# Kernel tuning notes

Measured on AMD Instinct MI355X. Metric: run time of the kernel, lower is better.

## Reference

```python
import jax, jax.numpy as jnp
import numpy as np

N = 20000      # total nodes
E = 320000     # edges before self loops
G = 64         # graphs in the batch
H = 8          # attention heads
NEG_SLOPE = 0.2
EPS = 1e-5


def _gatv2(x, src, dst, Wl, bl, Wr, br, att, bias, concat):
    # PyG GATv2Conv: xl = lin_l(x) (source/messages), xr = lin_r(x) (target)
    heads, C = att.shape
    xl = (x @ Wl + bl).reshape(-1, heads, C)
    xr = (x @ Wr + br).reshape(-1, heads, C)
    e = jax.nn.leaky_relu(xl[src] + xr[dst], NEG_SLOPE)          # [E', H, C]
    a = jnp.einsum('ehc,hc->eh', e, att)                          # [E', H]
    amax = jax.ops.segment_max(a, dst, num_segments=N)
    a = jnp.exp(a - amax[dst])
    a = a / jax.ops.segment_sum(a, dst, num_segments=N)[dst]
    out = jax.ops.segment_sum(xl[src] * a[..., None], dst, num_segments=N)
    out = out.reshape(-1, heads * C) if concat else out.mean(axis=1)
    return out + bias


def _graphnorm(x, batch, w, b, ms):
    cnt = jnp.maximum(jax.ops.segment_sum(jnp.ones((x.shape[0],), x.dtype), batch, num_segments=G), 1.0)[:, None]
    mean = jax.ops.segment_sum(x, batch, num_segments=G) / cnt
    out = x - mean[batch] * ms
    var = jax.ops.segment_sum(out * out, batch, num_segments=G) / cnt
    return w * out / jnp.sqrt(var + EPS)[batch] + b


def _mean_pool(x, batch):
    cnt = jnp.maximum(jax.ops.segment_sum(jnp.ones((x.shape[0],), x.dtype), batch, num_segments=G), 1.0)[:, None]
    return jax.ops.segment_sum(x, batch, num_segments=G) / cnt


def setup_inputs():
    key = jax.random.key(0)
    ks = iter(jax.random.split(key, 40))

    def gl(shape, scale=0.05):
        return jax.random.normal(next(ks), shape, jnp.float32) * scale

    inp = {}
    inp['x'] = jax.random.normal(next(ks), (N, 19), jnp.float32)
    inp['edge_index'] = jax.random.randint(next(ks), (2, E), 0, N, jnp.int32)
    inp['batch'] = jnp.sort(jax.random.randint(next(ks), (N,), 0, G, jnp.int32))

    # layer 1: 19 -> (8 heads x 32), concat -> 256
    inp['W1l'] = gl((19, 256)); inp['b1l'] = jnp.zeros((256,), jnp.float32)
    inp['W1r'] = gl((19, 256)); inp['b1r'] = jnp.zeros((256,), jnp.float32)
    inp['att1'] = gl((H, 32)); inp['bias1'] = jnp.zeros((256,), jnp.float32)
    inp['gn1_w'] = jnp.ones((256,), jnp.float32); inp['gn1_b'] = jnp.zeros((256,), jnp.float32); inp['gn1_ms'] = jnp.ones((256,), jnp.float32)

    inp['W2l'] = gl((256, 128)); inp['b2l'] = jnp.zeros((128,), jnp.float32)
    inp['W2r'] = gl((256, 128)); inp['b2r'] = jnp.zeros((128,), jnp.float32)
    inp['att2'] = gl((H, 16)); inp['bias2'] = jnp.zeros((128,), jnp.float32)
    inp['gn2_w'] = jnp.ones((128,), jnp.float32); inp['gn2_b'] = jnp.zeros((128,), jnp.float32); inp['gn2_ms'] = jnp.ones((128,), jnp.float32)

    inp['W3l'] = gl((128, 64)); inp['b3l'] = jnp.zeros((64,), jnp.float32)
    inp['W3r'] = gl((128, 64)); inp['b3r'] = jnp.zeros((64,), jnp.float32)
    inp['att3'] = gl((H, 8)); inp['bias3'] = jnp.zeros((8,), jnp.float32)
    inp['gn3_w'] = jnp.ones((8,), jnp.float32); inp['gn3_b'] = jnp.zeros((8,), jnp.float32); inp['gn3_ms'] = jnp.ones((8,), jnp.float32)

    inp['lin_w'] = gl((8, 4)); inp['lin_b'] = jnp.zeros((4,), jnp.float32)
    return inp


def reference(x, edge_index, batch, W1l, b1l, W1r, b1r, att1, bias1, gn1_w, gn1_b, gn1_ms,
              W2l, b2l, W2r, b2r, att2, bias2, gn2_w, gn2_b, gn2_ms,
              W3l, b3l, W3r, b3r, att3, bias3, gn3_w, gn3_b, gn3_ms, lin_w, lin_b):
    loop = jnp.arange(N, dtype=edge_index.dtype)  # GATv2Conv add_self_loops=True
    src = jnp.concatenate([edge_index[0], loop])
    dst = jnp.concatenate([edge_index[1], loop])

    h = _gatv2(x, src, dst, W1l, b1l, W1r, b1r, att1, bias1, True)
    h = jax.nn.relu(_graphnorm(h, batch, gn1_w, gn1_b, gn1_ms))
    h = _gatv2(h, src, dst, W2l, b2l, W2r, b2r, att2, bias2, True)
    h = jax.nn.relu(_graphnorm(h, batch, gn2_w, gn2_b, gn2_ms))
    h = _gatv2(h, src, dst, W3l, b3l, W3r, b3r, att3, bias3, False)
    h = jax.nn.relu(_graphnorm(h, batch, gn3_w, gn3_b, gn3_ms))

    features = _mean_pool(h, batch)        # [G, 8]
    logits = features @ lin_w + lin_b      # [G, 4]
    return (logits, features)
```

## Files before the change

kernel.cpp:

```cpp
#include <hip/hip_runtime.h>
#include <math.h>

#define NN 20000
#define EE 320000
#define GG 64
#define HH 8
#define EPSV 1e-5f

static inline unsigned int gridFor(long n, int b){ return (unsigned int)((n + b - 1)/b); }

typedef __attribute__((ext_vector_type(8))) short short8;
typedef __attribute__((ext_vector_type(4))) float f32x4;
typedef unsigned short ushort_t;

__global__ void k_deg(const int* __restrict__ edst, int* __restrict__ deg){
    int e = blockIdx.x*blockDim.x + threadIdx.x;
    if (e < EE) atomicAdd(&deg[edst[e]], 1);
}

__global__ void k_scan(const int* __restrict__ deg, int* __restrict__ indptr){
    __shared__ int partial[1024];
    const int CH = (NN + 1023)/1024;
    int t = threadIdx.x;
    int base = t*CH;
    int vals[CH];
    int sum = 0;
    for (int i = 0; i < CH; ++i){
        int v = (base+i < NN) ? deg[base+i] : 0;
        vals[i] = sum; sum += v;
    }
    partial[t] = sum;
    __syncthreads();
    for (int off = 1; off < 1024; off <<= 1){
        int v = (t >= off) ? partial[t-off] : 0;
        __syncthreads();
        partial[t] += v;
        __syncthreads();
    }
    int prefix = (t > 0) ? partial[t-1] : 0;
    for (int i = 0; i < CH; ++i)
        if (base+i < NN) indptr[base+i] = prefix + vals[i];
    if (t == 1023) indptr[NN] = prefix + sum;
}

__global__ void k_scatter(const int* __restrict__ esrc, const int* __restrict__ edst,
                          const int* __restrict__ indptr, int* __restrict__ cursor,
                          int* __restrict__ srclist){
    int e = blockIdx.x*blockDim.x + threadIdx.x;
    if (e >= EE) return;
    int d = edst[e];
    int pos = atomicAdd(&cursor[d], 1);
    srclist[indptr[d] + pos] = esrc[e];
}

__global__ void k_bounds(const int* __restrict__ batch, int* __restrict__ gstart, int* __restrict__ gend){
    int i = blockIdx.x*blockDim.x + threadIdx.x;
    if (i >= NN) return;
    int b = batch[i];
    if (i == 0 || batch[i-1] != b) gstart[b] = i;
    if (i == NN-1 || batch[i+1] != b) gend[b] = i+1;
}

__device__ __forceinline__ float asf(unsigned int u){
    union{unsigned int i; float f;} c; c.i = u; return c.f;
}
__device__ __forceinline__ ushort_t f2bf(float x){
    unsigned u = __float_as_uint(x);
    unsigned r = u + 0x7FFFu + ((u >> 16) & 1u);
    return (ushort_t)(r >> 16);
}
__device__ __forceinline__ void split_bf16(float x, short& hi, short& lo){
    unsigned u = __float_as_uint(x);
    unsigned r = u + 0x7FFFu + ((u >> 16) & 1u);
    hi = (short)(r >> 16);
    float hf = asf(((unsigned)(unsigned short)hi) << 16);
    float res = x - hf;
    unsigned u2 = __float_as_uint(res);
    unsigned r2 = u2 + 0x7FFFu + ((u2 >> 16) & 1u);
    lo = (short)(r2 >> 16);
}

__global__ void k_wprep(const float* __restrict__ Wl, const float* __restrict__ Wr,
                        ushort_t* __restrict__ Whi, ushort_t* __restrict__ Wlo,
                        int K, int Kp, int HC){
    int octs = Kp >> 3;
    int t = blockIdx.x*blockDim.x + threadIdx.x;
    if (t >= 2*HC*octs) return;
    int n = t / octs, ko = t - n*octs;
    int kb = ko*8;
    const float* W = (n < HC) ? (Wl + n) : (Wr + (n - HC));
    short hi[8], lo[8];
    #pragma unroll
    for (int j = 0; j < 8; ++j){
        int k = kb + j;
        float v = (k < K) ? W[(long)k*HC] : 0.f;
        split_bf16(v, hi[j], lo[j]);
    }
    long base = (((long)(n>>4)*(Kp>>5) + (kb>>5))*64 + (n&15) + 16*((kb>>3)&3))*8;
    *(short8*)&Whi[base] = *(short8*)hi;
    *(short8*)&Wlo[base] = *(short8*)lo;
}

template<bool NORM>
__global__ __launch_bounds__(256)
void k_gemm_mfma(const float* __restrict__ h,
                 const ushort_t* __restrict__ Whi, const ushort_t* __restrict__ Wlo,
                 const float* __restrict__ bl, const float* __restrict__ br,
                 const float* __restrict__ gmu, const float* __restrict__ ginv,
                 const float* __restrict__ nw, const float* __restrict__ nb,
                 const int* __restrict__ batch,
                 ushort_t* __restrict__ xlb, float* __restrict__ xr,
                 int K, int Kp, int HC){
    __shared__ short Ahi[64*32], Alo[64*32];
    const int tid  = threadIdx.x;
    const int lane = tid & 63;
    const int wave = tid >> 6;
    const int m0   = blockIdx.x * 64;
    const int n0   = blockIdx.y * 128;
    const int wr   = (wave & 1) * 32;
    const int wcg  = (wave >> 1) * 64;
    const int kblocks = Kp >> 5;

    const int srow = tid >> 2;
    const int soct = tid & 3;

    f32x4 acc[2][4] = {};

    for (int kb = 0; kb < kblocks; ++kb){
        int k0 = kb*32;
        {
            int gm = m0 + srow;
            int kbase = k0 + soct*8;
            float v[8];
            const float* src = h + (long)gm*K + kbase;
            if (gm < NN && kbase + 8 <= K){
                float4 t0 = *(const float4*)src;
                float4 t1 = *(const float4*)(src+4);
                v[0]=t0.x; v[1]=t0.y; v[2]=t0.z; v[3]=t0.w;
                v[4]=t1.x; v[5]=t1.y; v[6]=t1.z; v[7]=t1.w;
            } else {
                #pragma unroll
                for (int j = 0; j < 8; ++j)
                    v[j] = (gm < NN && kbase + j < K) ? src[j] : 0.f;
            }
            if (NORM && gm < NN){
                int g = batch[gm];
                const float* mu = gmu + (long)g*K;
                const float* iv = ginv + (long)g*K;
                #pragma unroll
                for (int j = 0; j < 8; ++j){
                    int c = kbase + j;
                    float t = (v[j] - mu[c]) * iv[c] * nw[c] + nb[c];
                    v[j] = fmaxf(t, 0.f);
                }
            }
            short hi[8], lo[8];
            #pragma unroll
            for (int j = 0; j < 8; ++j) split_bf16(v[j], hi[j], lo[j]);
            long off = ((long)(srow>>4)*64 + (srow&15) + 16*soct)*8;
            *(short8*)&Ahi[off] = *(short8*)hi;
            *(short8*)&Alo[off] = *(short8*)lo;
        }
        __syncthreads();

        int rb0 = wr >> 4;
        short8 ah0 = *(short8*)&Ahi[((rb0  )*64 + lane)*8];
        short8 ah1 = *(short8*)&Ahi[((rb0+1)*64 + lane)*8];
        short8 al0 = *(short8*)&Alo[((rb0  )*64 + lane)*8];
        short8 al1 = *(short8*)&Alo[((rb0+1)*64 + lane)*8];

        short8 bh[4], bl_[4];
        #pragma unroll
        for (int j = 0; j < 4; ++j){
            int n = n0 + wcg + j*16;
            long bbase = (((long)(n>>4)*kblocks + kb)*64 + lane)*8;
            bh[j]  = *(const short8*)&Whi[bbase];
            bl_[j] = *(const short8*)&Wlo[bbase];
        }

        #pragma unroll
        for (int j = 0; j < 4; ++j){
            acc[0][j] = __builtin_amdgcn_mfma_f32_16x16x32_bf16(al0, bh[j],  acc[0][j], 0,0,0);
            acc[0][j] = __builtin_amdgcn_mfma_f32_16x16x32_bf16(ah0, bl_[j], acc[0][j], 0,0,0);
            acc[0][j] = __builtin_amdgcn_mfma_f32_16x16x32_bf16(ah0, bh[j],  acc[0][j], 0,0,0);
            acc[1][j] = __builtin_amdgcn_mfma_f32_16x16x32_bf16(al1, bh[j],  acc[1][j], 0,0,0);
            acc[1][j] = __builtin_amdgcn_mfma_f32_16x16x32_bf16(ah1, bl_[j], acc[1][j], 0,0,0);
            acc[1][j] = __builtin_amdgcn_mfma_f32_16x16x32_bf16(ah1, bh[j],  acc[1][j], 0,0,0);
        }
        __syncthreads();
    }

    #pragma unroll
    for (int i = 0; i < 2; ++i){
        int row0 = m0 + wr + i*16 + (lane >> 4)*4;
        #pragma unroll
        for (int j = 0; j < 4; ++j){
            int n = n0 + wcg + j*16 + (lane & 15);
            float bb = (n < HC) ? bl[n] : br[n - HC];
            #pragma unroll
            for (int r = 0; r < 4; ++r){
                int gm = row0 + r;
                if (gm >= NN) continue;
                float v = acc[i][j][r] + bb;
                if (n < HC) xlb[(long)gm*HC + n] = f2bf(v);
                else        xr[(long)gm*HC + (n - HC)] = v;
            }
        }
    }
}

template<int VEC> struct VT;
template<> struct VT<1>{ using T = float;  };
template<> struct VT<2>{ using T = float2; };
template<> struct VT<4>{ using T = float4; };

template<int VEC> struct BF;
template<> struct BF<1>{
    static __device__ __forceinline__ float load(const ushort_t* p){
        return asf(((unsigned)*p) << 16);
    }
};
template<> struct BF<2>{
    static __device__ __forceinline__ float2 load(const ushort_t* p){
        unsigned u = *(const unsigned*)p;
        return make_float2(asf(u << 16), asf(u & 0xFFFF0000u));
    }
};
template<> struct BF<4>{
    static __device__ __forceinline__ float4 load(const ushort_t* p){
        uint2 u = *(const uint2*)p;
        return make_float4(asf(u.x << 16), asf(u.x & 0xFFFF0000u),
                           asf(u.y << 16), asf(u.y & 0xFFFF0000u));
    }
};

__device__ __forceinline__ float lrelu(float z){ return z > 0.f ? z : 0.2f*z; }

__device__ __forceinline__ float edot(float xv, float xr, float at){
    return lrelu(xv + xr) * at;
}
__device__ __forceinline__ float edot(float2 xv, float2 xr, float2 at){
    return lrelu(xv.x+xr.x)*at.x + lrelu(xv.y+xr.y)*at.y;
}
__device__ __forceinline__ float edot(float4 xv, float4 xr, float4 at){
    return lrelu(xv.x+xr.x)*at.x + lrelu(xv.y+xr.y)*at.y
         + lrelu(xv.z+xr.z)*at.z + lrelu(xv.w+xr.w)*at.w;
}
__device__ __forceinline__ void efma(float& o, float p, float xv){ o = fmaf(p,xv,o); }
__device__ __forceinline__ void efma(float2& o, float p, float2 xv){
    o.x = fmaf(p,xv.x,o.x); o.y = fmaf(p,xv.y,o.y);
}
__device__ __forceinline__ void efma(float4& o, float p, float4 xv){
    o.x = fmaf(p,xv.x,o.x); o.y = fmaf(p,xv.y,o.y);
    o.z = fmaf(p,xv.z,o.z); o.w = fmaf(p,xv.w,o.w);
}
__device__ __forceinline__ float escale(float o, float s, float b){ return fmaf(o,s,b); }
__device__ __forceinline__ float2 escale(float2 o, float s, float2 b){
    return make_float2(fmaf(o.x,s,b.x), fmaf(o.y,s,b.y));
}
__device__ __forceinline__ float4 escale(float4 o, float s, float4 b){
    return make_float4(fmaf(o.x,s,b.x), fmaf(o.y,s,b.y), fmaf(o.z,s,b.z), fmaf(o.w,s,b.w));
}

__device__ __forceinline__ float red8(float v){
    v += __shfl_xor(v, 1);
    v += __shfl_xor(v, 2);
    v += __shfl_xor(v, 4);
    return v;
}

template<int VEC, bool MEAN>
__global__ __launch_bounds__(256)
void k_gat_w(const int* __restrict__ indptr, const int* __restrict__ srclist,
             const ushort_t* __restrict__ xlb, const float* __restrict__ xr,
             const float* __restrict__ att, const float* __restrict__ bias,
             float* __restrict__ val){
    using V = typename VT<VEC>::T;
    constexpr int HC = 64*VEC;
    const int lane = threadIdx.x & 63;
    const int d = blockIdx.x*4 + (threadIdx.x >> 6);
    const int co = lane*VEC;

    V xrd = *(const V*)&xr[(long)d*HC + co];
    V at  = *(const V*)&att[co];
    V xls = BF<VEC>::load(xlb + (long)d*HC + co);

    float m0 = red8(edot(xls, xrd, at));
    float l = 1.0f;
    V o = xls;

    int j = indptr[d], end = indptr[d+1];
    for (; j + 8 <= end; j += 8){
        int s0 = srclist[j+0], s1 = srclist[j+1], s2 = srclist[j+2], s3 = srclist[j+3];
        int s4 = srclist[j+4], s5 = srclist[j+5], s6 = srclist[j+6], s7 = srclist[j+7];
        V x0 = BF<VEC>::load(xlb + (long)s0*HC + co);
        V x1 = BF<VEC>::load(xlb + (long)s1*HC + co);
        V x2 = BF<VEC>::load(xlb + (long)s2*HC + co);
        V x3 = BF<VEC>::load(xlb + (long)s3*HC + co);
        V x4 = BF<VEC>::load(xlb + (long)s4*HC + co);
        V x5 = BF<VEC>::load(xlb + (long)s5*HC + co);
        V x6 = BF<VEC>::load(xlb + (long)s6*HC + co);
        V x7 = BF<VEC>::load(xlb + (long)s7*HC + co);
        float a0 = red8(edot(x0, xrd, at));
        float a1 = red8(edot(x1, xrd, at));
        float a2 = red8(edot(x2, xrd, at));
        float a3 = red8(edot(x3, xrd, at));
        float a4 = red8(edot(x4, xrd, at));
        float a5 = red8(edot(x5, xrd, at));
        float a6 = red8(edot(x6, xrd, at));
        float a7 = red8(edot(x7, xrd, at));
        float p0 = __expf(a0 - m0), p1 = __expf(a1 - m0);
        float p2 = __expf(a2 - m0), p3 = __expf(a3 - m0);
        float p4 = __expf(a4 - m0), p5 = __expf(a5 - m0);
        float p6 = __expf(a6 - m0), p7 = __expf(a7 - m0);
        l += ((p0+p1)+(p2+p3)) + ((p4+p5)+(p6+p7));
        efma(o, p0, x0); efma(o, p1, x1); efma(o, p2, x2); efma(o, p3, x3);
        efma(o, p4, x4); efma(o, p5, x5); efma(o, p6, x6); efma(o, p7, x7);
    }
    for (; j < end; j += 4){
        int m = end - j;
        int s0 = srclist[j];
        int s1 = (m > 1) ? srclist[j+1] : s0;
        int s2 = (m > 2) ? srclist[j+2] : s0;
        int s3 = (m > 3) ? srclist[j+3] : s0;
        V x0 = BF<VEC>::load(xlb + (long)s0*HC + co);
        V x1 = BF<VEC>::load(xlb + (long)s1*HC + co);
        V x2 = BF<VEC>::load(xlb + (long)s2*HC + co);
        V x3 = BF<VEC>::load(xlb + (long)s3*HC + co);
        float a0 = red8(edot(x0, xrd, at));
        float a1 = red8(edot(x1, xrd, at));
        float a2 = red8(edot(x2, xrd, at));
        float a3 = red8(edot(x3, xrd, at));
        float p0 = __expf(a0 - m0);
        float p1 = __expf(a1 - m0);
        float p2 = __expf(a2 - m0);
        float p3 = __expf(a3 - m0);
        l += p0; efma(o, p0, x0);
        if (m > 1){ l += p1; efma(o, p1, x1); }
        if (m > 2){ l += p2; efma(o, p2, x2); }
        if (m > 3){ l += p3; efma(o, p3, x3); }
    }
    float invl = 1.0f / l;
    if (!MEAN){
        V bv = *(const V*)&bias[co];
        *(V*)&val[(long)d*HC + co] = escale(o, invl, bv);
    } else {
        float r = ((float&)o) * invl;
        r += __shfl_xor(r, 8);
        r += __shfl_xor(r, 16);
        r += __shfl_xor(r, 32);
        if (lane < 8) val[(long)d*8 + lane] = r*0.125f + bias[lane];
    }
}

template<int F>
__global__ void k_gn_partial(const float* __restrict__ val,
                             const int* __restrict__ gstart, const int* __restrict__ gend,
                             float* __restrict__ gsum, float* __restrict__ gsq){
    int g = blockIdx.x, ch = blockIdx.y, nch = gridDim.y;
    int c = threadIdx.x;
    int s = gstart[g], e = gend[g];
    float sum = 0.f, sq = 0.f;
    for (int i = s + ch; i < e; i += nch){
        float v = val[(long)i*F + c];
        sum += v; sq += v*v;
    }
    if (sum != 0.f || sq != 0.f){
        atomicAdd(&gsum[g*F + c], sum);
        atomicAdd(&gsq[g*F + c], sq);
    }
}

__global__ void k_gn_finalize(const float* __restrict__ gsum, const float* __restrict__ gsq,
                              const int* __restrict__ gstart, const int* __restrict__ gend,
                              const float* __restrict__ ms,
                              float* __restrict__ gmu, float* __restrict__ ginv, int F){
    int idx = blockIdx.x*blockDim.x + threadIdx.x;
    if (idx >= GG*F) return;
    int g = idx / F, c = idx - g*F;
    int cnti = gend[g] - gstart[g];
    float cn = cnti > 0 ? (float)cnti : 1.f;
    float mean = gsum[idx] / cn;
    float mu = mean * ms[c];
    float var = gsq[idx]/cn - 2.f*mu*mean + mu*mu;
    gmu[idx]  = mu;
    ginv[idx] = rsqrtf(var + EPSV);
}

__global__ void k_gn_stats8(const float* __restrict__ val,
                            const int* __restrict__ gstart, const int* __restrict__ gend,
                            const float* __restrict__ ms,
                            float* __restrict__ gmu, float* __restrict__ ginv){
    const int F = 8;
    int g = blockIdx.x;
    int t = threadIdx.x;
    int c = t % F, r = t / F;
    int s = gstart[g], e = gend[g];
    float sum = 0.f, sq = 0.f;
    for (int i = s + r; i < e; i += 8){
        float v = val[(long)i*F + c];
        sum += v; sq += v*v;
    }
    #pragma unroll
    for (int mask = 8; mask < 64; mask <<= 1){
        sum += __shfl_xor(sum, mask, 64);
        sq  += __shfl_xor(sq,  mask, 64);
    }
    if (r == 0){
        int cnti = e - s;
        float cn = cnti > 0 ? (float)cnti : 1.f;
        float mean = sum / cn;
        float mu = mean * ms[c];
        float var = sq/cn - 2.f*mu*mean + mu*mu;
        gmu[g*F + c]  = mu;
        ginv[g*F + c] = rsqrtf(var + EPSV);
    }
}

__global__ void k_pool_gn(const float* __restrict__ D,
                          const int* __restrict__ gstart, const int* __restrict__ gend,
                          const float* __restrict__ gmu, const float* __restrict__ ginv,
                          const float* __restrict__ w, const float* __restrict__ b,
                          float* __restrict__ outFeat){
    int g = blockIdx.x;
    int t = threadIdx.x;
    int c = t & 7, r = t >> 3;
    int s = gstart[g], e = gend[g];
    float mu = gmu[g*8 + c], iv = ginv[g*8 + c], wc = w[c], bc = b[c];
    float sum = 0.f;
    for (int i = s + r; i < e; i += 8){
        float v = (D[(long)i*8 + c] - mu) * iv * wc + bc;
        sum += fmaxf(v, 0.f);
    }
    sum += __shfl_xor(sum, 8, 64);
    sum += __shfl_xor(sum, 16, 64);
    sum += __shfl_xor(sum, 32, 64);
    if (t < 8){
        int cnti = e - s;
        float cn = cnti > 0 ? (float)cnti : 1.f;
        outFeat[g*8 + t] = sum / cn;
    }
}

__global__ void k_logits(const float* __restrict__ feat, const float* __restrict__ lw,
                         const float* __restrict__ lb, float* __restrict__ outLog){
    int idx = blockIdx.x*blockDim.x + threadIdx.x;
    if (idx >= GG*4) return;
    int g = idx >> 2, j = idx & 3;
    float a = lb[j];
    for (int c = 0; c < 8; ++c) a += feat[g*8 + c] * lw[c*4 + j];
    outLog[idx] = a;
}

extern "C" void kernel_launch(void* const* d_in, const int* in_sizes, int n_in,
                              void* d_out, int out_size, void* d_ws, size_t ws_size,
                              hipStream_t stream) {
    const float* x     = (const float*)d_in[0];
    const int*   ei    = (const int*)  d_in[1];
    const int*   batch = (const int*)  d_in[2];
    const float* W1l = (const float*)d_in[3];  const float* b1l = (const float*)d_in[4];
    const float* W1r = (const float*)d_in[5];  const float* b1r = (const float*)d_in[6];
    const float* att1= (const float*)d_in[7];  const float* bias1=(const float*)d_in[8];
    const float* g1w = (const float*)d_in[9];  const float* g1b = (const float*)d_in[10];
    const float* g1m = (const float*)d_in[11];
    const float* W2l = (const float*)d_in[12]; const float* b2l = (const float*)d_in[13];
    const float* W2r = (const float*)d_in[14]; const float* b2r = (const float*)d_in[15];
    const float* att2= (const float*)d_in[16]; const float* bias2=(const float*)d_in[17];
    const float* g2w = (const float*)d_in[18]; const float* g2b = (const float*)d_in[19];
    const float* g2m = (const float*)d_in[20];
    const float* W3l = (const float*)d_in[21]; const float* b3l = (const float*)d_in[22];
    const float* W3r = (const float*)d_in[23]; const float* b3r = (const float*)d_in[24];
    const float* att3= (const float*)d_in[25]; const float* bias3=(const float*)d_in[26];
    const float* g3w = (const float*)d_in[27]; const float* g3b = (const float*)d_in[28];
    const float* g3m = (const float*)d_in[29];
    const float* lin_w=(const float*)d_in[30]; const float* lin_b=(const float*)d_in[31];

    const int* esrc = ei;
    const int* edst = ei + EE;

    float* ws = (float*)d_ws;
    int*   cursor  = (int*)(ws + 0);
    int*   indptr  = (int*)(ws + 20480);
    int*   srclist = (int*)(ws + 40960);
    int*   gstart  = (int*)(ws + 361472);
    int*   gend    = (int*)(ws + 361984);
    float* gmu     = ws + 362496;
    float* ginv    = ws + 378880;
    float* gsumP   = ws + 395264;
    float* gsqP    = ws + 411648;
    ushort_t* W1hi = (ushort_t*)(ws + 428032);
    ushort_t* W1lo = (ushort_t*)(ws + 436224);
    ushort_t* W2hi = (ushort_t*)(ws + 444416);
    ushort_t* W2lo = (ushort_t*)(ws + 477184);
    ushort_t* W3hi = (ushort_t*)(ws + 509952);
    ushort_t* W3lo = (ushort_t*)(ws + 518144);
    ushort_t* Bb = (ushort_t*)(ws + 526336);
    float* Cb = ws + 3086336;
    float* D  = ws + 8206336;

    const int TB = 256;
    const int MBm = (NN + 63)/64;
    const int NCH = 32;

    k_wprep<<<gridFor(512*4,  TB), TB, 0, stream>>>(W1l, W1r, W1hi, W1lo, 19, 32, 256);
    k_wprep<<<gridFor(256*32, TB), TB, 0, stream>>>(W2l, W2r, W2hi, W2lo, 256, 256, 128);
    k_wprep<<<gridFor(128*16, TB), TB, 0, stream>>>(W3l, W3r, W3hi, W3lo, 128, 128, 64);

    hipMemsetAsync(cursor, 0, NN*sizeof(int), stream);
    k_deg<<<gridFor(EE, TB), TB, 0, stream>>>(edst, cursor);
    k_scan<<<1, 1024, 0, stream>>>(cursor, indptr);
    hipMemsetAsync(cursor, 0, NN*sizeof(int), stream);
    k_scatter<<<gridFor(EE, TB), TB, 0, stream>>>(esrc, edst, indptr, cursor, srclist);
    k_bounds<<<gridFor(NN, TB), TB, 0, stream>>>(batch, gstart, gend);

    k_gemm_mfma<false><<<dim3(MBm, 4), 256, 0, stream>>>(x, W1hi, W1lo, b1l, b1r,
        nullptr, nullptr, nullptr, nullptr, nullptr, Bb, Cb, 19, 32, 256);
    k_gat_w<4, false><<<NN/4, 256, 0, stream>>>(indptr, srclist, Bb, Cb, att1, bias1, D);
    hipMemsetAsync(gsumP, 0, 2*GG*256*sizeof(float), stream);
    k_gn_partial<256><<<dim3(GG, NCH), 256, 0, stream>>>(D, gstart, gend, gsumP, gsqP);
    k_gn_finalize<<<gridFor(GG*256, TB), TB, 0, stream>>>(gsumP, gsqP, gstart, gend, g1m, gmu, ginv, 256);

    k_gemm_mfma<true><<<dim3(MBm, 2), 256, 0, stream>>>(D, W2hi, W2lo, b2l, b2r,
        gmu, ginv, g1w, g1b, batch, Bb, Cb, 256, 256, 128);
    k_gat_w<2, false><<<NN/4, 256, 0, stream>>>(indptr, srclist, Bb, Cb, att2, bias2, D);
    hipMemsetAsync(gsumP, 0, 2*GG*256*sizeof(float), stream);
    k_gn_partial<128><<<dim3(GG, NCH), 128, 0, stream>>>(D, gstart, gend, gsumP, gsqP);
    k_gn_finalize<<<gridFor(GG*128, TB), TB, 0, stream>>>(gsumP, gsqP, gstart, gend, g2m, gmu, ginv, 128);

    k_gemm_mfma<true><<<dim3(MBm, 1), 256, 0, stream>>>(D, W3hi, W3lo, b3l, b3r,
        gmu, ginv, g2w, g2b, batch, Bb, Cb, 128, 128, 64);
    k_gat_w<1, true><<<NN/4, 256, 0, stream>>>(indptr, srclist, Bb, Cb, att3, bias3, D);
    k_gn_stats8<<<GG, 64, 0, stream>>>(D, gstart, gend, g3m, gmu, ginv);

    float* outLog  = (float*)d_out;
    float* outFeat = outLog + GG*4;
    k_pool_gn<<<GG, 64, 0, stream>>>(D, gstart, gend, gmu, ginv, g3w, g3b, outFeat);
    k_logits<<<1, 256, 0, stream>>>(outFeat, lin_w, lin_b, outLog);
}
```

Before: 345.4 us.

## Fuse setup, memsets and tail kernels; double-buffer GEMM LDS tiles

Merges the three weight-prep kernels and the cursor memset into one launch. Folds degree counting, graph bounds and the GN accumulator zeroing into one kernel, and moves the other resets into k_scan and k_gn_finalize. Fuses the final GN stats, pooling and logits into one tail kernel. It also double-buffers the GEMM A tile in shared memory so one barrier per k-step can be dropped. The aim is to cut launch and memset overhead across about seven fewer launches, at the cost of more complex reset ordering.

```diff
diff --git a/kernel.cpp b/kernel.cpp
--- a/kernel.cpp
+++ b/kernel.cpp
@@ -13,12 +13,77 @@
 typedef __attribute__((ext_vector_type(4))) float f32x4;
 typedef unsigned short ushort_t;
 
-__global__ void k_deg(const int* __restrict__ edst, int* __restrict__ deg){
+__device__ __forceinline__ float asf(unsigned int u){
+    union{unsigned int i; float f;} c; c.i = u; return c.f;
+}
+__device__ __forceinline__ ushort_t f2bf(float x){
+    unsigned u = __float_as_uint(x);
+    unsigned r = u + 0x7FFFu + ((u >> 16) & 1u);
+    return (ushort_t)(r >> 16);
+}
+__device__ __forceinline__ void split_bf16(float x, short& hi, short& lo){
+    unsigned u = __float_as_uint(x);
+    unsigned r = u + 0x7FFFu + ((u >> 16) & 1u);
+    hi = (short)(r >> 16);
+    float hf = asf(((unsigned)(unsigned short)hi) << 16);
+    float res = x - hf;
+    unsigned u2 = __float_as_uint(res);
+    unsigned r2 = u2 + 0x7FFFu + ((u2 >> 16) & 1u);
+    lo = (short)(r2 >> 16);
+}
+
+__device__ __forceinline__ void wprep_one(const float* Wl, const float* Wr,
+                                          ushort_t* Whi, ushort_t* Wlo,
+                                          int K, int Kp, int HC, int t){
+    int octs = Kp >> 3;
+    int n = t / octs, ko = t - n*octs;
+    int kb = ko*8;
+    const float* W = (n < HC) ? (Wl + n) : (Wr + (n - HC));
+    short hi[8], lo[8];
+    #pragma unroll
+    for (int j = 0; j < 8; ++j){
+        int k = kb + j;
+        float v = (k < K) ? W[(long)k*HC] : 0.f;
+        split_bf16(v, hi[j], lo[j]);
+    }
+    long base = (((long)(n>>4)*(Kp>>5) + (kb>>5))*64 + (n&15) + 16*((kb>>3)&3))*8;
+    *(short8*)&Whi[base] = *(short8*)hi;
+    *(short8*)&Wlo[base] = *(short8*)lo;
+}
+
+#define WP1 2048
+#define WP2 8192
+#define WP3 2048
+
+__global__ void k_wprep_all(const float* __restrict__ W1l, const float* __restrict__ W1r,
+                            const float* __restrict__ W2l, const float* __restrict__ W2r,
+                            const float* __restrict__ W3l, const float* __restrict__ W3r,
+                            ushort_t* __restrict__ W1hi, ushort_t* __restrict__ W1lo,
+                            ushort_t* __restrict__ W2hi, ushort_t* __restrict__ W2lo,
+                            ushort_t* __restrict__ W3hi, ushort_t* __restrict__ W3lo,
+                            int* __restrict__ cursor){
+    int t = blockIdx.x*blockDim.x + threadIdx.x;
+    if (t < NN) cursor[t] = 0;
+    if (t < WP1) wprep_one(W1l, W1r, W1hi, W1lo, 19, 32, 256, t);
+    else if (t < WP1+WP2) wprep_one(W2l, W2r, W2hi, W2lo, 256, 256, 128, t-WP1);
+    else if (t < WP1+WP2+WP3) wprep_one(W3l, W3r, W3hi, W3lo, 128, 128, 64, t-WP1-WP2);
+}
+
+__global__ void k_degbounds(const int* __restrict__ edst, int* __restrict__ deg,
+                            const int* __restrict__ batch,
+                            int* __restrict__ gstart, int* __restrict__ gend,
+                            float* __restrict__ gz){
     int e = blockIdx.x*blockDim.x + threadIdx.x;
     if (e < EE) atomicAdd(&deg[edst[e]], 1);
-}
-
-__global__ void k_scan(const int* __restrict__ deg, int* __restrict__ indptr){
+    if (e < NN){
+        int b = batch[e];
+        if (e == 0 || batch[e-1] != b) gstart[b] = e;
+        if (e == NN-1 || batch[e+1] != b) gend[b] = e+1;
+    }
+    if (e < 2*GG*256) gz[e] = 0.f;
+}
+
+__global__ void k_scan(int* __restrict__ deg, int* __restrict__ indptr){
     __shared__ int partial[1024];
     const int CH = (NN + 1023)/1024;
     int t = threadIdx.x;
@@ -29,6 +94,8 @@
         int v = (base+i < NN) ? deg[base+i] : 0;
         vals[i] = sum; sum += v;
     }
+    for (int i = 0; i < CH; ++i)
+        if (base+i < NN) deg[base+i] = 0;
     partial[t] = sum;
     __syncthreads();
     for (int off = 1; off < 1024; off <<= 1){
@@ -51,54 +118,6 @@
     int d = edst[e];
     int pos = atomicAdd(&cursor[d], 1);
     srclist[indptr[d] + pos] = esrc[e];
-}
-
-__global__ void k_bounds(const int* __restrict__ batch, int* __restrict__ gstart, int* __restrict__ gend){
-    int i = blockIdx.x*blockDim.x + threadIdx.x;
-    if (i >= NN) return;
-    int b = batch[i];
-    if (i == 0 || batch[i-1] != b) gstart[b] = i;
-    if (i == NN-1 || batch[i+1] != b) gend[b] = i+1;
-}
-
-__device__ __forceinline__ float asf(unsigned int u){
-    union{unsigned int i; float f;} c; c.i = u; return c.f;
-}
-__device__ __forceinline__ ushort_t f2bf(float x){
-    unsigned u = __float_as_uint(x);
-    unsigned r = u + 0x7FFFu + ((u >> 16) & 1u);
-    return (ushort_t)(r >> 16);
-}
-__device__ __forceinline__ void split_bf16(float x, short& hi, short& lo){
-    unsigned u = __float_as_uint(x);
-    unsigned r = u + 0x7FFFu + ((u >> 16) & 1u);
-    hi = (short)(r >> 16);
-    float hf = asf(((unsigned)(unsigned short)hi) << 16);
-    float res = x - hf;
-    unsigned u2 = __float_as_uint(res);
-    unsigned r2 = u2 + 0x7FFFu + ((u2 >> 16) & 1u);
-    lo = (short)(r2 >> 16);
-}
-
-__global__ void k_wprep(const float* __restrict__ Wl, const float* __restrict__ Wr,
-                        ushort_t* __restrict__ Whi, ushort_t* __restrict__ Wlo,
-                        int K, int Kp, int HC){
-    int octs = Kp >> 3;
-    int t = blockIdx.x*blockDim.x + threadIdx.x;
-    if (t >= 2*HC*octs) return;
-    int n = t / octs, ko = t - n*octs;
-    int kb = ko*8;
-    const float* W = (n < HC) ? (Wl + n) : (Wr + (n - HC));
-    short hi[8], lo[8];
-    #pragma unroll
-    for (int j = 0; j < 8; ++j){
-        int k = kb + j;
-        float v = (k < K) ? W[(long)k*HC] : 0.f;
-        split_bf16(v, hi[j], lo[j]);
-    }
-    long base = (((long)(n>>4)*(Kp>>5) + (kb>>5))*64 + (n&15) + 16*((kb>>3)&3))*8;
-    *(short8*)&Whi[base] = *(short8*)hi;
-    *(short8*)&Wlo[base] = *(short8*)lo;
 }
 
 template<bool NORM>
@@ -111,7 +130,7 @@
                  const int* __restrict__ batch,
                  ushort_t* __restrict__ xlb, float* __restrict__ xr,
                  int K, int Kp, int HC){
-    __shared__ short Ahi[64*32], Alo[64*32];
+    __shared__ short Ahi[2][64*32], Alo[2][64*32];
     const int tid  = threadIdx.x;
     const int lane = tid & 63;
     const int wave = tid >> 6;
@@ -127,6 +146,7 @@
     f32x4 acc[2][4] = {};
 
     for (int kb = 0; kb < kblocks; ++kb){
+        int p = kb & 1;
         int k0 = kb*32;
         {
             int gm = m0 + srow;
@@ -158,16 +178,16 @@
             #pragma unroll
             for (int j = 0; j < 8; ++j) split_bf16(v[j], hi[j], lo[j]);
             long off = ((long)(srow>>4)*64 + (srow&15) + 16*soct)*8;
-            *(short8*)&Ahi[off] = *(short8*)hi;
-            *(short8*)&Alo[off] = *(short8*)lo;
+            *(short8*)&Ahi[p][off] = *(short8*)hi;
+            *(short8*)&Alo[p][off] = *(short8*)lo;
         }
         __syncthreads();
 
         int rb0 = wr >> 4;
-        short8 ah0 = *(short8*)&Ahi[((rb0  )*64 + lane)*8];
-        short8 ah1 = *(short8*)&Ahi[((rb0+1)*64 + lane)*8];
-        short8 al0 = *(short8*)&Alo[((rb0  )*64 + lane)*8];
-        short8 al1 = *(short8*)&Alo[((rb0+1)*64 + lane)*8];
+        short8 ah0 = *(short8*)&Ahi[p][((rb0  )*64 + lane)*8];
+        short8 ah1 = *(short8*)&Ahi[p][((rb0+1)*64 + lane)*8];
+        short8 al0 = *(short8*)&Alo[p][((rb0  )*64 + lane)*8];
+        short8 al1 = *(short8*)&Alo[p][((rb0+1)*64 + lane)*8];
 
         short8 bh[4], bl_[4];
         #pragma unroll
@@ -187,7 +207,6 @@
             acc[1][j] = __builtin_amdgcn_mfma_f32_16x16x32_bf16(ah1, bl_[j], acc[1][j], 0,0,0);
             acc[1][j] = __builtin_amdgcn_mfma_f32_16x16x32_bf16(ah1, bh[j],  acc[1][j], 0,0,0);
         }
-        __syncthreads();
     }
 
     #pragma unroll
@@ -371,7 +390,7 @@
     }
 }
 
-__global__ void k_gn_finalize(const float* __restrict__ gsum, const float* __restrict__ gsq,
+__global__ void k_gn_finalize(float* __restrict__ gsum, float* __restrict__ gsq,
                               const int* __restrict__ gstart, const int* __restrict__ gend,
                               const float* __restrict__ ms,
                               float* __restrict__ gmu, float* __restrict__ ginv, int F){
@@ -385,20 +404,26 @@
     float var = gsq[idx]/cn - 2.f*mu*mean + mu*mu;
     gmu[idx]  = mu;
     ginv[idx] = rsqrtf(var + EPSV);
-}
-
-__global__ void k_gn_stats8(const float* __restrict__ val,
-                            const int* __restrict__ gstart, const int* __restrict__ gend,
-                            const float* __restrict__ ms,
-                            float* __restrict__ gmu, float* __restrict__ ginv){
-    const int F = 8;
+    gsum[idx] = 0.f;
+    gsq[idx]  = 0.f;
+}
+
+__global__ void k_tail(const float* __restrict__ D,
+                       const int* __restrict__ gstart, const int* __restrict__ gend,
+                       const float* __restrict__ ms, const float* __restrict__ w,
+                       const float* __restrict__ b,
+                       const float* __restrict__ lw, const float* __restrict__ lb,
+                       float* __restrict__ outLog, float* __restrict__ outFeat){
     int g = blockIdx.x;
     int t = threadIdx.x;
-    int c = t % F, r = t / F;
+    int c = t & 7, r = t >> 3;
     int s = gstart[g], e = gend[g];
+    int cnti = e - s;
+    float cn = cnti > 0 ? (float)cnti : 1.f;
+
     float sum = 0.f, sq = 0.f;
     for (int i = s + r; i < e; i += 8){
-        float v = val[(long)i*F + c];
+        float v = D[(long)i*8 + c];
         sum += v; sq += v*v;
     }
     #pragma unroll
@@ -406,50 +431,35 @@
         sum += __shfl_xor(sum, mask, 64);
         sq  += __shfl_xor(sq,  mask, 64);
     }
-    if (r == 0){
-        int cnti = e - s;
-        float cn = cnti > 0 ? (float)cnti : 1.f;
-        float mean = sum / cn;
-        float mu = mean * ms[c];
-        float var = sq/cn - 2.f*mu*mean + mu*mu;
-        gmu[g*F + c]  = mu;
-        ginv[g*F + c] = rsqrtf(var + EPSV);
-    }
-}
-
-__global__ void k_pool_gn(const float* __restrict__ D,
-                          const int* __restrict__ gstart, const int* __restrict__ gend,
-                          const float* __restrict__ gmu, const float* __restrict__ ginv,
-                          const float* __restrict__ w, const float* __restrict__ b,
-                          float* __restrict__ outFeat){
-    int g = blockIdx.x;
-    int t = threadIdx.x;
-    int c = t & 7, r = t >> 3;
-    int s = gstart[g], e = gend[g];
-    float mu = gmu[g*8 + c], iv = ginv[g*8 + c], wc = w[c], bc = b[c];
-    float sum = 0.f;
+    float mean = sum / cn;
+    float mu = mean * ms[c];
+    float var = sq/cn - 2.f*mu*mean + mu*mu;
+    float iv = rsqrtf(var + EPSV);
+    float wc = w[c], bc = b[c];
+
+    float psum = 0.f;
     for (int i = s + r; i < e; i += 8){
         float v = (D[(long)i*8 + c] - mu) * iv * wc + bc;
-        sum += fmaxf(v, 0.f);
-    }
-    sum += __shfl_xor(sum, 8, 64);
-    sum += __shfl_xor(sum, 16, 64);
-    sum += __shfl_xor(sum, 32, 64);
-    if (t < 8){
-        int cnti = e - s;
-        float cn = cnti > 0 ? (float)cnti : 1.f;
-        outFeat[g*8 + t] = sum / cn;
-    }
-}
-
-__global__ void k_logits(const float* __restrict__ feat, const float* __restrict__ lw,
-                         const float* __restrict__ lb, float* __restrict__ outLog){
-    int idx = blockIdx.x*blockDim.x + threadIdx.x;
-    if (idx >= GG*4) return;
-    int g = idx >> 2, j = idx & 3;
-    float a = lb[j];
-    for (int c = 0; c < 8; ++c) a += feat[g*8 + c] * lw[c*4 + j];
-    outLog[idx] = a;
+        psum += fmaxf(v, 0.f);
+    }
+    #pragma unroll
+    for (int mask = 8; mask < 64; mask <<= 1)
+        psum += __shfl_xor(psum, mask, 64);
+    float feat = psum / cn;
+
+    if (t < 8) outFeat[g*8 + t] = feat;
+
+    float a = 0.f;
+    int jj = t;
+    if (t < 4){
+        a = lb[jj];
+    }
+    #pragma unroll
+    for (int cc = 0; cc < 8; ++cc){
+        float fc = __shfl(feat, cc, 64);
+        if (t < 4) a += fc * lw[cc*4 + jj];
+    }
+    if (t < 4) outLog[g*4 + jj] = a;
 }
 
 extern "C" void kernel_launch(void* const* d_in, const int* in_sizes, int n_in,
@@ -502,38 +512,29 @@
     const int MBm = (NN + 63)/64;
     const int NCH = 32;
 
-    k_wprep<<<gridFor(512*4,  TB), TB, 0, stream>>>(W1l, W1r, W1hi, W1lo, 19, 32, 256);
-    k_wprep<<<gridFor(256*32, TB), TB, 0, stream>>>(W2l, W2r, W2hi, W2lo, 256, 256, 128);
-    k_wprep<<<gridFor(128*16, TB), TB, 0, stream>>>(W3l, W3r, W3hi, W3lo, 128, 128, 64);
-
-    hipMemsetAsync(cursor, 0, NN*sizeof(int), stream);
-    k_deg<<<gridFor(EE, TB), TB, 0, stream>>>(edst, cursor);
+    k_wprep_all<<<gridFor(NN, TB), TB, 0, stream>>>(W1l, W1r, W2l, W2r, W3l, W3r,
+        W1hi, W1lo, W2hi, W2lo, W3hi, W3lo, cursor);
+    k_degbounds<<<gridFor(EE, TB), TB, 0, stream>>>(edst, cursor, batch, gstart, gend, gsumP);
     k_scan<<<1, 1024, 0, stream>>>(cursor, indptr);
-    hipMemsetAsync(cursor, 0, NN*sizeof(int), stream);
     k_scatter<<<gridFor(EE, TB), TB, 0, stream>>>(esrc, edst, indptr, cursor, srclist);
-    k_bounds<<<gridFor(NN, TB), TB, 0, stream>>>(batch, gstart, gend);
 
     k_gemm_mfma<false><<<dim3(MBm, 4), 256, 0, stream>>>(x, W1hi, W1lo, b1l, b1r,
         nullptr, nullptr, nullptr, nullptr, nullptr, Bb, Cb, 19, 32, 256);
     k_gat_w<4, false><<<NN/4, 256, 0, stream>>>(indptr, srclist, Bb, Cb, att1, bias1, D);
-    hipMemsetAsync(gsumP, 0, 2*GG*256*sizeof(float), stream);
     k_gn_partial<256><<<dim3(GG, NCH), 256, 0, stream>>>(D, gstart, gend, gsumP, gsqP);
     k_gn_finalize<<<gridFor(GG*256, TB), TB, 0, stream>>>(gsumP, gsqP, gstart, gend, g1m, gmu, ginv, 256);
 
     k_gemm_mfma<true><<<dim3(MBm, 2), 256, 0, stream>>>(D, W2hi, W2lo, b2l, b2r,
         gmu, ginv, g1w, g1b, batch, Bb, Cb, 256, 256, 128);
     k_gat_w<2, false><<<NN/4, 256, 0, stream>>>(indptr, srclist, Bb, Cb, att2, bias2, D);
-    hipMemsetAsync(gsumP, 0, 2*GG*256*sizeof(float), stream);
     k_gn_partial<128><<<dim3(GG, NCH), 128, 0, stream>>>(D, gstart, gend, gsumP, gsqP);
     k_gn_finalize<<<gridFor(GG*128, TB), TB, 0, stream>>>(gsumP, gsqP, gstart, gend, g2m, gmu, ginv, 128);
 
     k_gemm_mfma<true><<<dim3(MBm, 1), 256, 0, stream>>>(D, W3hi, W3lo, b3l, b3r,
         gmu, ginv, g2w, g2b, batch, Bb, Cb, 128, 128, 64);
     k_gat_w<1, true><<<NN/4, 256, 0, stream>>>(indptr, srclist, Bb, Cb, att3, bias3, D);
-    k_gn_stats8<<<GG, 64, 0, stream>>>(D, gstart, gend, g3m, gmu, ginv);
 
     float* outLog  = (float*)d_out;
     float* outFeat = outLog + GG*4;
-    k_pool_gn<<<GG, 64, 0, stream>>>(D, gstart, gend, gmu, ginv, g3w, g3b, outFeat);
-    k_logits<<<1, 256, 0, stream>>>(outFeat, lin_w, lin_b, outLog);
-}
+    k_tail<<<GG, 64, 0, stream>>>(D, gstart, gend, g3m, g3w, g3b, lin_w, lin_b, outLog, outFeat);
+}
```

After: 344.7 us. About the same (-0.2%).
